# Optimization experiments

Measured on AMD Instinct MI355X. Metric: run time of the kernel, lower is better.

The kernel has to match this reference:

```python
import jax, jax.numpy as jnp
import numpy as np

MODEL_DIM = 1024
NUM_HEADS = 16
K_DIM = MODEL_DIM // NUM_HEADS


def setup_inputs() -> dict:
    key = jax.random.key(0)
    kx, kw1, kw2 = jax.random.split(key, 3)
    B, L, D = 4, 2048, MODEL_DIM
    x = jax.random.normal(kx, (B, L, D), dtype=jnp.float32)
    # nn.Linear(D, 3D, bias=False): y = x @ W^T; store transposed form [D, 3D]
    scale1 = 1.0 / np.sqrt(D)
    Wqkv = jax.random.uniform(kw1, (D, 3 * D), dtype=jnp.float32, minval=-scale1, maxval=scale1)
    Wout = jax.random.uniform(kw2, (D, D), dtype=jnp.float32, minval=-scale1, maxval=scale1)
    return {"x": x, "Wqkv": Wqkv, "Wout": Wout}


def reference(x, Wqkv, Wout):
    B, L, D = x.shape
    H, Kd = NUM_HEADS, K_DIM
    qkv = x @ Wqkv  # [B, L, 3D]
    q, k, v = jnp.split(qkv, 3, axis=-1)

    def heads(t):  # [B, L, D] -> [B, H, L, Kd]
        return t.reshape(B, L, H, Kd).transpose(0, 2, 1, 3)

    qh, kh, vh = heads(q), heads(k), heads(v)
    scores = jnp.einsum('bhqd,bhkd->bhqk', qh, kh) / jnp.sqrt(jnp.float32(Kd))
    causal = jnp.triu(jnp.ones((L, L), dtype=bool), k=1)  # True above diagonal
    scores = jnp.where(causal, -jnp.inf, scores)
    probs = jax.nn.softmax(scores, axis=-1)
    attended = jnp.einsum('bhqk,bhkd->bhqd', probs, vh)
    concatted = attended.transpose(0, 2, 1, 3).reshape(B, L, D)
    # dropout is identity in eval mode
    return concatted @ Wout
```

## Files before the change

kernel.cpp:

```cpp
#include <hip/hip_runtime.h>

typedef unsigned short u16;
typedef unsigned int   u32;
typedef __bf16   bf16x8 __attribute__((ext_vector_type(8)));
typedef float    f32x4  __attribute__((ext_vector_type(4)));
typedef u16      u16x4  __attribute__((ext_vector_type(4)));
typedef u16      u16x8  __attribute__((ext_vector_type(8)));
typedef u32      u32x2  __attribute__((ext_vector_type(2)));
typedef u32      u32x4  __attribute__((ext_vector_type(4)));

#if __has_builtin(__builtin_amdgcn_exp2f)
#define EXP2(x) __builtin_amdgcn_exp2f(x)
#else
#define EXP2(x) exp2f(x)
#endif

__device__ __forceinline__ u16 f2bf(float f) {
    unsigned u = __float_as_uint(f);
    u += 0x7FFFu + ((u >> 16) & 1u);
    return (u16)(u >> 16);
}

__device__ __forceinline__ u32 pack_bf16(float a, float b) {
#if __has_builtin(__builtin_amdgcn_cvt_pk_bf16_f32)
    typedef __bf16 bf16x2 __attribute__((ext_vector_type(2)));
    bf16x2 r = __builtin_amdgcn_cvt_pk_bf16_f32(a, b);
    return __builtin_bit_cast(u32, r);
#else
    return (u32)f2bf(a) | ((u32)f2bf(b) << 16);
#endif
}

__device__ __forceinline__ void async_copy16(const u16* g, u16* l) {
    __builtin_amdgcn_global_load_lds(
        (const __attribute__((address_space(1))) unsigned*)g,
        (__attribute__((address_space(3))) unsigned*)l, 16, 0, 0);
}

__device__ __forceinline__ bf16x8 lds_frag(const u16* p) {
    return *(const bf16x8*)p;
}

__device__ __forceinline__ void permlane32_swap(u32& a, u32& b) {
    asm("v_permlane32_swap_b32 %0, %1" : "+v"(a), "+v"(b));
}
__device__ __forceinline__ void permlane16_swap(u32& a, u32& b) {
    asm("v_permlane16_swap_b32 %0, %1" : "+v"(a), "+v"(b));
}

__global__ __launch_bounds__(256) void prep(const float* __restrict__ x,
                                            const float* __restrict__ Wqkv,
                                            const float* __restrict__ Wout,
                                            u16* __restrict__ xb,
                                            u16* __restrict__ wqkv_t,
                                            u16* __restrict__ wout_t) {
    __shared__ u16 t[64 * 72];
    const int bid = blockIdx.x;
    const int tid = threadIdx.x;

    if (bid >= 1024) {
        size_t i = ((size_t)(bid - 1024) * 256 + tid) * 8;
        float4 v0 = *(const float4*)(x + i);
        float4 v1 = *(const float4*)(x + i + 4);
        u16x8 o = { f2bf(v0.x), f2bf(v0.y), f2bf(v0.z), f2bf(v0.w),
                    f2bf(v1.x), f2bf(v1.y), f2bf(v1.z), f2bf(v1.w) };
        *(u16x8*)(xb + i) = o;
        return;
    }

    const float* W;  u16* Wt;  int Kd, Nd, n0, k0;
    if (bid < 768) { W = Wqkv; Wt = wqkv_t; Kd = 1024; Nd = 3072;
                     n0 = (bid % 48) * 64; k0 = (bid / 48) * 64; }
    else           { W = Wout; Wt = wout_t; Kd = 1024; Nd = 1024;
                     n0 = ((bid - 768) % 16) * 64; k0 = ((bid - 768) / 16) * 64; }
#pragma unroll
    for (int i = 0; i < 4; ++i) {
        int lin = i * 256 + tid;
        int kr = lin >> 4, nc = (lin & 15) << 2;
        float4 v = *(const float4*)(W + (size_t)(k0 + kr) * Nd + n0 + nc);
        u16x4 o = { f2bf(v.x), f2bf(v.y), f2bf(v.z), f2bf(v.w) };
        *(u16x4*)&t[kr * 72 + nc] = o;
    }
    __syncthreads();
#pragma unroll
    for (int i = 0; i < 2; ++i) {
        int lin = i * 256 + tid;
        int nr = lin >> 3, kc = (lin & 7) << 3;
        u16x8 o;
#pragma unroll
        for (int jj = 0; jj < 8; ++jj) o[jj] = t[(kc + jj) * 72 + nr];
        *(u16x8*)(Wt + (size_t)(n0 + nr) * Kd + k0 + kc) = o;
    }
}

__global__ __launch_bounds__(256) void gemm_qkv(const u16* __restrict__ A,
                                                const u16* __restrict__ Bt,
                                                u16* __restrict__ outb,
                                                int K, int N) {
    __shared__ u16 As[2][128 * 32];
    __shared__ u16 Bs[2][128 * 32];
    const int tid = threadIdx.x;
    const int lane = tid & 63;
    const int wv = tid >> 6;
    const int wr = (wv >> 1) * 64;
    const int wc = (wv & 1) * 64;
    const int qd = lane >> 4;
    const int c  = lane & 15;

    const int flat = blockIdx.x;
    const int r_ = flat & 7;
    const int q_ = flat >> 3;
    const int m0 = ((r_ >> 1) * 16 + q_ / 12) * 128;
    const int n0 = ((r_ & 1) * 12 + q_ % 12) * 128;

    const int srow = tid >> 2;
    const int sg = ((tid & 3) ^ ((srow >> 1) & 3)) << 3;

    const u16* Ag0 = A  + (size_t)(m0 +      srow) * K + sg;
    const u16* Ag1 = A  + (size_t)(m0 + 64 + srow) * K + sg;
    const u16* Bg0 = Bt + (size_t)(n0 +      srow) * K + sg;
    const u16* Bg1 = Bt + (size_t)(n0 + 64 + srow) * K + sg;

    const u32 fsw = (qd ^ ((c >> 1) & 3)) << 3;
    const u32 a_off = (wr + c) * 32 + fsw;
    const u32 b_off = (wc + c) * 32 + fsw;

    f32x4 acc[4][4] = {};

    async_copy16(Ag0, &As[0][tid * 8]);
    async_copy16(Ag1, &As[0][2048 + tid * 8]);
    async_copy16(Bg0, &Bs[0][tid * 8]);
    async_copy16(Bg1, &Bs[0][2048 + tid * 8]);

    int p = 0;
    for (int k0 = 0; k0 < K; k0 += 32) {
        __syncthreads();
        if (k0 + 32 < K) {
            const int np = p ^ 1;
            async_copy16(Ag0 + k0 + 32, &As[np][tid * 8]);
            async_copy16(Ag1 + k0 + 32, &As[np][2048 + tid * 8]);
            async_copy16(Bg0 + k0 + 32, &Bs[np][tid * 8]);
            async_copy16(Bg1 + k0 + 32, &Bs[np][2048 + tid * 8]);
        }
        bf16x8 af[4], bfr[4];
#pragma unroll
        for (int i = 0; i < 4; ++i) af[i]  = lds_frag(&As[p][a_off + i * 512]);
#pragma unroll
        for (int j = 0; j < 4; ++j) bfr[j] = lds_frag(&Bs[p][b_off + j * 512]);
#pragma unroll
        for (int i = 0; i < 4; ++i)
#pragma unroll
            for (int j = 0; j < 4; ++j)
                acc[i][j] = __builtin_amdgcn_mfma_f32_16x16x32_bf16(af[i], bfr[j], acc[i][j], 0, 0, 0);
        p ^= 1;
    }

#pragma unroll
    for (int i = 0; i < 4; ++i)
#pragma unroll
        for (int j = 0; j < 4; ++j) {
            int n = n0 + wc + j * 16 + c;
            int which = n >> 10, h = (n >> 6) & 15, kd = n & 63;
            int m_base = m0 + wr + i * 16 + qd * 4;
            int b = m_base >> 11, l0 = m_base & 2047;
            int bh = b * 16 + h;
            if (which == 2) {
                u32x2 o2;
                o2[0] = pack_bf16(acc[i][j][0], acc[i][j][1]);
                o2[1] = pack_bf16(acc[i][j][2], acc[i][j][3]);
                *(u32x2*)(outb + (size_t)(128 + bh) * 131072 + (size_t)kd * 2048 + l0) = o2;
            } else if (which == 0) {
#pragma unroll
                for (int r = 0; r < 4; ++r)
                    outb[(size_t)bh * 131072 + (size_t)(l0 + r) * 64 + kd] =
                        f2bf(acc[i][j][r] * 0.1803368801f);
            } else {
#pragma unroll
                for (int r = 0; r < 4; ++r)
                    outb[(size_t)(64 + bh) * 131072 + (size_t)(l0 + r) * 64 + kd] =
                        f2bf(acc[i][j][r]);
            }
        }
}

__global__ __launch_bounds__(256) void gemm_out(const u16* __restrict__ A,
                                                const u16* __restrict__ Bt,
                                                float* __restrict__ outf,
                                                int K, int N) {
    __shared__ u16 As[2][128 * 32];
    __shared__ u16 Bs[2][128 * 32];
    const int tid = threadIdx.x;
    const int lane = tid & 63;
    const int wv = tid >> 6;
    const int wr = (wv >> 1) * 64;
    const int wc = (wv & 1) * 64;
    const int qd = lane >> 4;
    const int c  = lane & 15;

    const int flat = blockIdx.x;
    const int r_ = flat & 7;
    const int q_ = flat >> 3;
    const int m0 = (r_ * 8 + (q_ >> 3)) * 128;
    const int n0 = (q_ & 7) * 128;

    const int srow = tid >> 2;
    const int sg = ((tid & 3) ^ ((srow >> 1) & 3)) << 3;

    const u16* Ag0 = A  + (size_t)(m0 +      srow) * K + sg;
    const u16* Ag1 = A  + (size_t)(m0 + 64 + srow) * K + sg;
    const u16* Bg0 = Bt + (size_t)(n0 +      srow) * K + sg;
    const u16* Bg1 = Bt + (size_t)(n0 + 64 + srow) * K + sg;

    const u32 fsw = (qd ^ ((c >> 1) & 3)) << 3;
    const u32 a_off = (wr + c) * 32 + fsw;
    const u32 b_off = (wc + c) * 32 + fsw;

    f32x4 acc[4][4] = {};

    async_copy16(Ag0, &As[0][tid * 8]);
    async_copy16(Ag1, &As[0][2048 + tid * 8]);
    async_copy16(Bg0, &Bs[0][tid * 8]);
    async_copy16(Bg1, &Bs[0][2048 + tid * 8]);

    int p = 0;
    for (int k0 = 0; k0 < K; k0 += 32) {
        __syncthreads();
        if (k0 + 32 < K) {
            const int np = p ^ 1;
            async_copy16(Ag0 + k0 + 32, &As[np][tid * 8]);
            async_copy16(Ag1 + k0 + 32, &As[np][2048 + tid * 8]);
            async_copy16(Bg0 + k0 + 32, &Bs[np][tid * 8]);
            async_copy16(Bg1 + k0 + 32, &Bs[np][2048 + tid * 8]);
        }
        bf16x8 af[4], bfr[4];
#pragma unroll
        for (int i = 0; i < 4; ++i) af[i]  = lds_frag(&As[p][a_off + i * 512]);
#pragma unroll
        for (int j = 0; j < 4; ++j) bfr[j] = lds_frag(&Bs[p][b_off + j * 512]);
#pragma unroll
        for (int i = 0; i < 4; ++i)
#pragma unroll
            for (int j = 0; j < 4; ++j)
                acc[i][j] = __builtin_amdgcn_mfma_f32_16x16x32_bf16(af[i], bfr[j], acc[i][j], 0, 0, 0);
        p ^= 1;
    }

#pragma unroll
    for (int i = 0; i < 4; ++i)
#pragma unroll
        for (int j = 0; j < 4; ++j) {
            int n = n0 + wc + j * 16 + c;
            int m_base = m0 + wr + i * 16 + qd * 4;
#pragma unroll
            for (int r = 0; r < 4; ++r)
                outf[(size_t)(m_base + r) * N + n] = acc[i][j][r];
        }
}

#define ATTN_S_AB(KSB)                                                        \
    do {                                                                      \
        _Pragma("unroll") for (int f = 0; f < 8; ++f) {                       \
            sa[f] = f32x4{-8.f, -8.f, -8.f, -8.f};                            \
            sb[f] = f32x4{-8.f, -8.f, -8.f, -8.f};                            \
        }                                                                     \
        __builtin_amdgcn_s_setprio(1);                                        \
        _Pragma("unroll") for (int ks = 0; ks < 2; ++ks) {                    \
            const u16* kp = (KSB) + kf_off[ks];                               \
            _Pragma("unroll") for (int f = 0; f < 8; ++f) {                   \
                bf16x8 kf = lds_frag(kp + f * 1024);                          \
                sa[f] = __builtin_amdgcn_mfma_f32_16x16x32_bf16(              \
                    kf, qa[ks], sa[f], 0, 0, 0);                              \
                sb[f] = __builtin_amdgcn_mfma_f32_16x16x32_bf16(              \
                    kf, qb[ks], sb[f], 0, 0, 0);                              \
            }                                                                 \
        }                                                                     \
        __builtin_amdgcn_s_setprio(0);                                        \
    } while (0)

#define ATTN_FINISH_AB(VTB, KT)                                               \
    do {                                                                      \
        if ((KT) == qt) {                                                     \
            _Pragma("unroll") for (int f = 0; f < 8; ++f)                     \
                _Pragma("unroll") for (int r = 0; r < 4; ++r) {               \
                    int key = (KT) * 128 + f * 16 + qd * 4 + r;               \
                    if (key > qa_row) sa[f][r] = -3e38f;                      \
                    if (key > qb_row) sb[f][r] = -3e38f;                      \
                }                                                             \
        }                                                                     \
        _Pragma("unroll") for (int f = 0; f < 8; ++f) {                       \
            _Pragma("unroll") for (int r = 0; r < 4; ++r) {                   \
                sa[f][r] = EXP2(sa[f][r]);                                    \
                sb[f][r] = EXP2(sb[f][r]);                                    \
            }                                                                 \
            rva += sa[f];                                                     \
            rvb += sb[f];                                                     \
        }                                                                     \
        _Pragma("unroll") for (int kc = 0; kc < 4; ++kc) {                    \
            u32 a0 = pack_bf16(sa[2 * kc][0], sa[2 * kc][1]);                 \
            u32 a1 = pack_bf16(sa[2 * kc + 1][0], sa[2 * kc + 1][1]);         \
            u32 b0 = pack_bf16(sa[2 * kc][2], sa[2 * kc][3]);                 \
            u32 b1 = pack_bf16(sa[2 * kc + 1][2], sa[2 * kc + 1][3]);         \
            permlane32_swap(a0, a1); permlane16_swap(a0, a1);                 \
            permlane32_swap(b0, b1); permlane16_swap(b0, b1);                 \
            u32x4 wpa = {a0, b0, a1, b1};                                     \
            bf16x8 pa = __builtin_bit_cast(bf16x8, wpa);                      \
            u32 c0 = pack_bf16(sb[2 * kc][0], sb[2 * kc][1]);                 \
            u32 c1 = pack_bf16(sb[2 * kc + 1][0], sb[2 * kc + 1][1]);         \
            u32 d0 = pack_bf16(sb[2 * kc][2], sb[2 * kc][3]);                 \
            u32 d1 = pack_bf16(sb[2 * kc + 1][2], sb[2 * kc + 1][3]);         \
            permlane32_swap(c0, c1); permlane16_swap(c0, c1);                 \
            permlane32_swap(d0, d1); permlane16_swap(d0, d1);                 \
            u32x4 wpb = {c0, d0, c1, d1};                                     \
            bf16x8 pb = __builtin_bit_cast(bf16x8, wpb);                      \
            const u16* vp = (VTB) + vf_off[kc];                               \
            __builtin_amdgcn_s_setprio(1);                                    \
            _Pragma("unroll") for (int jo = 0; jo < 4; ++jo) {                \
                bf16x8 vf = lds_frag(vp + jo * 2048);                         \
                acca[jo] = __builtin_amdgcn_mfma_f32_16x16x32_bf16(           \
                    vf, pa, acca[jo], 0, 0, 0);                               \
                accb[jo] = __builtin_amdgcn_mfma_f32_16x16x32_bf16(           \
                    vf, pb, accb[jo], 0, 0, 0);                               \
            }                                                                 \
            __builtin_amdgcn_s_setprio(0);                                    \
        }                                                                     \
    } while (0)

__global__ __launch_bounds__(256, 2) void attn_kernel(const u16* __restrict__ qkv,
                                                      u16* __restrict__ att) {
    __shared__ u16 Ks[2][128 * 64];
    __shared__ u16 Vt[2][64 * 128];

    const int tid = threadIdx.x;
    const int lane = tid & 63;
    const int w = tid >> 6;
    const int qd = lane >> 4;
    const int c = lane & 15;

    const int flat = blockIdx.x + 8 * blockIdx.y;
    const int bh = (flat & 7) + 8 * ((flat >> 3) & 7);
    const int bx = flat >> 6;
    const int b = bh >> 4, h = bh & 15;

    const u16* Qg = qkv + (size_t)bh * 131072;
    const u16* Kg = qkv + (size_t)(64 + bh) * 131072;
    const u16* Vg = qkv + (size_t)(128 + bh) * 131072;

    u32 kf_off[2];
#pragma unroll
    for (int ks = 0; ks < 2; ++ks)
        kf_off[ks] = c * 64 + (((ks * 4 + qd) ^ (c & 7)) << 3);
    u32 vf_off[4];
#pragma unroll
    for (int kc = 0; kc < 4; ++kc)
        vf_off[kc] = c * 128 + (((kc * 4 + qd) ^ c) << 3);

    auto issue_copy = [&](int t, u16* kd, u16* vd) {
#pragma unroll
        for (int it = 0; it < 4; ++it) {
            int lin = it * 256 + tid;
            int krw = lin >> 3, kch = lin & 7;
            int vrw = lin >> 4, vch = lin & 15;
            async_copy16(Kg + (size_t)t * 8192 + krw * 64 + ((kch ^ (krw & 7)) << 3),
                         kd + lin * 8);
            async_copy16(Vg + (size_t)t * 128 + (size_t)vrw * 2048 + ((vch ^ (vrw & 15)) << 3),
                         vd + lin * 8);
        }
    };

#pragma unroll 1
    for (int seg = 0; seg < 2; ++seg) {
        const int qt = seg ? (15 - bx) : bx;
        const int qa_row = qt * 128 + w * 32 + c;
        const int qb_row = qa_row + 16;

        bf16x8 qa[2], qb[2];
#pragma unroll
        for (int ks = 0; ks < 2; ++ks) {
            qa[ks] = *(const bf16x8*)(Qg + (size_t)qa_row * 64 + ks * 32 + qd * 8);
            qb[ks] = *(const bf16x8*)(Qg + (size_t)qb_row * 64 + ks * 32 + qd * 8);
        }

        f32x4 acca[4] = {}, accb[4] = {};
        f32x4 rva = {}, rvb = {};
        f32x4 sa[8], sb[8];

        const int nkt = qt + 1;

        __syncthreads();
        issue_copy(0, Ks[0], Vt[0]);
        __syncthreads();
        if (nkt > 1) issue_copy(1, Ks[1], Vt[1]);

#pragma unroll 1
        for (int kt = 0; kt < nkt; ++kt) {
            const int p = kt & 1;
            ATTN_S_AB(Ks[p]);
            ATTN_FINISH_AB(Vt[p], kt);
            if (kt + 1 < nkt) {
                __syncthreads();
                if (kt + 2 < nkt) issue_copy(kt + 2, Ks[p], Vt[p]);
            }
        }

        float ra = rva[0] + rva[1] + rva[2] + rva[3];
        float rb = rvb[0] + rvb[1] + rvb[2] + rvb[3];
        ra += __shfl_xor(ra, 16, 64);
        ra += __shfl_xor(ra, 32, 64);
        rb += __shfl_xor(rb, 16, 64);
        rb += __shfl_xor(rb, 32, 64);
        float ia = __builtin_amdgcn_rcpf(ra), ib = __builtin_amdgcn_rcpf(rb);
        u16* ar = att + ((size_t)b * 2048 + qa_row) * 1024 + h * 64;
        u16* br = att + ((size_t)b * 2048 + qb_row) * 1024 + h * 64;
#pragma unroll
        for (int jo = 0; jo < 4; ++jo) {
            u32x2 oa, ob;
            oa[0] = pack_bf16(acca[jo][0] * ia, acca[jo][1] * ia);
            oa[1] = pack_bf16(acca[jo][2] * ia, acca[jo][3] * ia);
            ob[0] = pack_bf16(accb[jo][0] * ib, accb[jo][1] * ib);
            ob[1] = pack_bf16(accb[jo][2] * ib, accb[jo][3] * ib);
            *(u32x2*)(ar + jo * 16 + qd * 4) = oa;
            *(u32x2*)(br + jo * 16 + qd * 4) = ob;
        }
    }
}

extern "C" void kernel_launch(void* const* d_in, const int* in_sizes, int n_in,
                              void* d_out, int out_size, void* d_ws, size_t ws_size,
                              hipStream_t stream) {
    const float* x    = (const float*)d_in[0];
    const float* Wqkv = (const float*)d_in[1];
    const float* Wout = (const float*)d_in[2];
    float* out = (float*)d_out;

    char* ws = (char*)d_ws;
    u16* x_bf   = (u16*)(ws);
    u16* wqkv_t = (u16*)(ws + 16777216);
    u16* wout_t = (u16*)(ws + 23068672);
    u16* qkv_h  = (u16*)(ws + 25165824);
    u16* att    = (u16*)(ws + 75497472);

    prep<<<dim3(5120), dim3(256), 0, stream>>>(x, Wqkv, Wout, x_bf, wqkv_t, wout_t);
    gemm_qkv<<<dim3(1536), dim3(256), 0, stream>>>(x_bf, wqkv_t, qkv_h, 1024, 3072);
    attn_kernel<<<dim3(8, 64), dim3(256), 0, stream>>>(qkv_h, att);
    gemm_out<<<dim3(512), dim3(256), 0, stream>>>(att, wout_t, out, 1024, 1024);
}
```

Measured before the change: 240.7 us.

## Share K/V tile loads across both query tiles in attention block

Restructures the attention kernel so each block streams K/V tiles once and applies them to both of its paired query tiles (bx and 15-bx), instead of running two sequential passes. This removes the duplicated global-to-LDS copies and barriers for the shared key range, as well as the second pipeline prologue. In exchange, each thread now holds two sets of Q fragments, output accumulators and row sums, which raises register pressure and may cause spills or lower occupancy.

```diff
diff --git a/kernel.cpp b/kernel.cpp
--- a/kernel.cpp
+++ b/kernel.cpp
@@ -257,7 +257,7 @@
         }
 }
 
-#define ATTN_S_AB(KSB)                                                        \
+#define ATTN_S(KSB, QA, QB)                                                   \
     do {                                                                      \
         _Pragma("unroll") for (int f = 0; f < 8; ++f) {                       \
             sa[f] = f32x4{-8.f, -8.f, -8.f, -8.f};                            \
@@ -269,22 +269,22 @@
             _Pragma("unroll") for (int f = 0; f < 8; ++f) {                   \
                 bf16x8 kf = lds_frag(kp + f * 1024);                          \
                 sa[f] = __builtin_amdgcn_mfma_f32_16x16x32_bf16(              \
-                    kf, qa[ks], sa[f], 0, 0, 0);                              \
+                    kf, QA[ks], sa[f], 0, 0, 0);                              \
                 sb[f] = __builtin_amdgcn_mfma_f32_16x16x32_bf16(              \
-                    kf, qb[ks], sb[f], 0, 0, 0);                              \
+                    kf, QB[ks], sb[f], 0, 0, 0);                              \
             }                                                                 \
         }                                                                     \
         __builtin_amdgcn_s_setprio(0);                                        \
     } while (0)
 
-#define ATTN_FINISH_AB(VTB, KT)                                               \
+#define ATTN_FIN(VTB, KT, QT, QAROW, QBROW, RVA, RVB, ACCA, ACCB)             \
     do {                                                                      \
-        if ((KT) == qt) {                                                     \
+        if ((KT) == (QT)) {                                                   \
             _Pragma("unroll") for (int f = 0; f < 8; ++f)                     \
                 _Pragma("unroll") for (int r = 0; r < 4; ++r) {               \
                     int key = (KT) * 128 + f * 16 + qd * 4 + r;               \
-                    if (key > qa_row) sa[f][r] = -3e38f;                      \
-                    if (key > qb_row) sb[f][r] = -3e38f;                      \
+                    if (key > (QAROW)) sa[f][r] = -3e38f;                     \
+                    if (key > (QBROW)) sb[f][r] = -3e38f;                     \
                 }                                                             \
         }                                                                     \
         _Pragma("unroll") for (int f = 0; f < 8; ++f) {                       \
@@ -292,8 +292,8 @@
                 sa[f][r] = EXP2(sa[f][r]);                                    \
                 sb[f][r] = EXP2(sb[f][r]);                                    \
             }                                                                 \
-            rva += sa[f];                                                     \
-            rvb += sb[f];                                                     \
+            RVA += sa[f];                                                     \
+            RVB += sb[f];                                                     \
         }                                                                     \
         _Pragma("unroll") for (int kc = 0; kc < 4; ++kc) {                    \
             u32 a0 = pack_bf16(sa[2 * kc][0], sa[2 * kc][1]);                 \
@@ -316,10 +316,10 @@
             __builtin_amdgcn_s_setprio(1);                                    \
             _Pragma("unroll") for (int jo = 0; jo < 4; ++jo) {                \
                 bf16x8 vf = lds_frag(vp + jo * 2048);                         \
-                acca[jo] = __builtin_amdgcn_mfma_f32_16x16x32_bf16(           \
-                    vf, pa, acca[jo], 0, 0, 0);                               \
-                accb[jo] = __builtin_amdgcn_mfma_f32_16x16x32_bf16(           \
-                    vf, pb, accb[jo], 0, 0, 0);                               \
+                ACCA[jo] = __builtin_amdgcn_mfma_f32_16x16x32_bf16(           \
+                    vf, pa, ACCA[jo], 0, 0, 0);                               \
+                ACCB[jo] = __builtin_amdgcn_mfma_f32_16x16x32_bf16(           \
+                    vf, pb, ACCB[jo], 0, 0, 0);                               \
             }                                                                 \
             __builtin_amdgcn_s_setprio(0);                                    \
         }                                                                     \
@@ -367,57 +367,71 @@
         }
     };
 
+    const int qt0 = bx;
+    const int qt1 = 15 - bx;
+    const int NT  = qt1 + 1;
+
+    const int qa0_row = qt0 * 128 + w * 32 + c;
+    const int qb0_row = qa0_row + 16;
+    const int qa1_row = qt1 * 128 + w * 32 + c;
+    const int qb1_row = qa1_row + 16;
+
+    bf16x8 qa0[2], qb0[2], qa1[2], qb1[2];
+#pragma unroll
+    for (int ks = 0; ks < 2; ++ks) {
+        qa0[ks] = *(const bf16x8*)(Qg + (size_t)qa0_row * 64 + ks * 32 + qd * 8);
+        qb0[ks] = *(const bf16x8*)(Qg + (size_t)qb0_row * 64 + ks * 32 + qd * 8);
+        qa1[ks] = *(const bf16x8*)(Qg + (size_t)qa1_row * 64 + ks * 32 + qd * 8);
+        qb1[ks] = *(const bf16x8*)(Qg + (size_t)qb1_row * 64 + ks * 32 + qd * 8);
+    }
+
+    f32x4 aa0[4] = {}, ab0[4] = {}, aa1[4] = {}, ab1[4] = {};
+    f32x4 rva0 = {}, rvb0 = {}, rva1 = {}, rvb1 = {};
+    f32x4 sa[8], sb[8];
+
+    issue_copy(0, Ks[0], Vt[0]);
+    __syncthreads();
+    if (NT > 1) issue_copy(1, Ks[1], Vt[1]);
+
 #pragma unroll 1
-    for (int seg = 0; seg < 2; ++seg) {
-        const int qt = seg ? (15 - bx) : bx;
-        const int qa_row = qt * 128 + w * 32 + c;
-        const int qb_row = qa_row + 16;
-
-        bf16x8 qa[2], qb[2];
-#pragma unroll
-        for (int ks = 0; ks < 2; ++ks) {
-            qa[ks] = *(const bf16x8*)(Qg + (size_t)qa_row * 64 + ks * 32 + qd * 8);
-            qb[ks] = *(const bf16x8*)(Qg + (size_t)qb_row * 64 + ks * 32 + qd * 8);
-        }
-
-        f32x4 acca[4] = {}, accb[4] = {};
-        f32x4 rva = {}, rvb = {};
-        f32x4 sa[8], sb[8];
-
-        const int nkt = qt + 1;
-
-        __syncthreads();
-        issue_copy(0, Ks[0], Vt[0]);
-        __syncthreads();
-        if (nkt > 1) issue_copy(1, Ks[1], Vt[1]);
-
-#pragma unroll 1
-        for (int kt = 0; kt < nkt; ++kt) {
-            const int p = kt & 1;
-            ATTN_S_AB(Ks[p]);
-            ATTN_FINISH_AB(Vt[p], kt);
-            if (kt + 1 < nkt) {
-                __syncthreads();
-                if (kt + 2 < nkt) issue_copy(kt + 2, Ks[p], Vt[p]);
-            }
-        }
-
-        float ra = rva[0] + rva[1] + rva[2] + rva[3];
-        float rb = rvb[0] + rvb[1] + rvb[2] + rvb[3];
+    for (int kt = 0; kt < NT; ++kt) {
+        const int p = kt & 1;
+        if (kt <= qt0) {
+            ATTN_S(Ks[p], qa0, qb0);
+            ATTN_FIN(Vt[p], kt, qt0, qa0_row, qb0_row, rva0, rvb0, aa0, ab0);
+        }
+        ATTN_S(Ks[p], qa1, qb1);
+        ATTN_FIN(Vt[p], kt, qt1, qa1_row, qb1_row, rva1, rvb1, aa1, ab1);
+        if (kt + 1 < NT) {
+            __syncthreads();
+            if (kt + 2 < NT) issue_copy(kt + 2, Ks[p], Vt[p]);
+        }
+    }
+
+#pragma unroll
+    for (int sgi = 0; sgi < 2; ++sgi) {
+        f32x4* Aa = sgi ? aa1 : aa0;
+        f32x4* Ab = sgi ? ab1 : ab0;
+        f32x4 rv_a = sgi ? rva1 : rva0;
+        f32x4 rv_b = sgi ? rvb1 : rvb0;
+        int ra_row = sgi ? qa1_row : qa0_row;
+        int rb_row = sgi ? qb1_row : qb0_row;
+        float ra = rv_a[0] + rv_a[1] + rv_a[2] + rv_a[3];
+        float rb = rv_b[0] + rv_b[1] + rv_b[2] + rv_b[3];
         ra += __shfl_xor(ra, 16, 64);
         ra += __shfl_xor(ra, 32, 64);
         rb += __shfl_xor(rb, 16, 64);
         rb += __shfl_xor(rb, 32, 64);
         float ia = __builtin_amdgcn_rcpf(ra), ib = __builtin_amdgcn_rcpf(rb);
-        u16* ar = att + ((size_t)b * 2048 + qa_row) * 1024 + h * 64;
-        u16* br = att + ((size_t)b * 2048 + qb_row) * 1024 + h * 64;
+        u16* ar = att + ((size_t)b * 2048 + ra_row) * 1024 + h * 64;
+        u16* br = att + ((size_t)b * 2048 + rb_row) * 1024 + h * 64;
 #pragma unroll
         for (int jo = 0; jo < 4; ++jo) {
             u32x2 oa, ob;
-            oa[0] = pack_bf16(acca[jo][0] * ia, acca[jo][1] * ia);
-            oa[1] = pack_bf16(acca[jo][2] * ia, acca[jo][3] * ia);
-            ob[0] = pack_bf16(accb[jo][0] * ib, accb[jo][1] * ib);
-            ob[1] = pack_bf16(accb[jo][2] * ib, accb[jo][3] * ib);
+            oa[0] = pack_bf16(Aa[jo][0] * ia, Aa[jo][1] * ia);
+            oa[1] = pack_bf16(Aa[jo][2] * ia, Aa[jo][3] * ia);
+            ob[0] = pack_bf16(Ab[jo][0] * ib, Ab[jo][1] * ib);
+            ob[1] = pack_bf16(Ab[jo][2] * ib, Ab[jo][3] * ib);
             *(u32x2*)(ar + jo * 16 + qd * 4) = oa;
             *(u32x2*)(br + jo * 16 + qd * 4) = ob;
         }
```

Measured after the change: 239.1 us. About the same (-0.7%).
